# Optimization experiments

Measured on AMD Instinct MI355X. Metric: run time of the kernel, lower is better.

Reference implementation:

```python
import jax, jax.numpy as jnp
import numpy as np

HEAD_SIZE = 64
SCALE = HEAD_SIZE ** -0.5


def setup_inputs() -> dict:
    key = jax.random.key(0)
    ks = jax.random.split(key, 7)
    B, T, E, H = 32, 2048, 1024, HEAD_SIZE
    x = jax.random.normal(ks[0], (B, T, E), dtype=jnp.float32)
    Wq = jax.random.normal(ks[1], (E, H), dtype=jnp.float32) * (E ** -0.5)
    bq = jax.random.normal(ks[2], (H,), dtype=jnp.float32) * 0.02
    Wk = jax.random.normal(ks[3], (E, H), dtype=jnp.float32) * (E ** -0.5)
    bk = jax.random.normal(ks[4], (H,), dtype=jnp.float32) * 0.02
    Wv = jax.random.normal(ks[5], (E, H), dtype=jnp.float32) * (E ** -0.5)
    bv = jax.random.normal(ks[6], (H,), dtype=jnp.float32) * 0.02
    return {"x": x, "Wq": Wq, "bq": bq, "Wk": Wk, "bk": bk, "Wv": Wv, "bv": bv}


def reference(x, Wq, bq, Wk, bk, Wv, bv):
    # Faithful to the torch source: the tril buffer is all ones so the mask is a
    # no-op, and F.softmax's result is discarded. Output = (Q K^T * scale) @ V.
    Q = x @ Wq + bq          # [B, T, H]
    K = x @ Wk + bk          # [B, T, H]
    V = x @ Wv + bv          # [B, T, H]
    wei = jnp.einsum('bqh,bkh->bqk', Q, K) * SCALE  # [B, T, T]
    return jnp.einsum('bqk,bkh->bqh', wei, V)       # [B, T, H]
```

## Files before the change

### kernel.cpp

```cpp
#include <hip/hip_runtime.h>
#include <hip/hip_bf16.h>


using bf16x8 = __attribute__((ext_vector_type(8))) short;
using f32x4  = __attribute__((ext_vector_type(4))) float;
using u32x4  = __attribute__((ext_vector_type(4))) unsigned int;
using u32x2  = __attribute__((ext_vector_type(2))) unsigned int;
using u16    = unsigned short;

__device__ __forceinline__ u16 f2bf(float f) {
    unsigned u = __builtin_bit_cast(unsigned, f);
    u += 0x7fffu + ((u >> 16) & 1u);
    return (u16)(u >> 16);
}
__device__ __forceinline__ float bflo(unsigned u) { return __builtin_bit_cast(float, u << 16); }
__device__ __forceinline__ float bfhi(unsigned u) { return __builtin_bit_cast(float, u & 0xffff0000u); }

#define G2L16(g, l) __builtin_amdgcn_global_load_lds(                         \
    (const __attribute__((address_space(1))) void*)(g),                       \
    (__attribute__((address_space(3))) void*)(l), 16, 0, 0)

__global__ __launch_bounds__(256) void k_wt(const float* __restrict__ Wq,
                                            const float* __restrict__ Wk,
                                            const float* __restrict__ Wv,
                                            u16* __restrict__ WT) {
    const int n = blockIdx.x;
    const int seg = n >> 6, col = n & 63;
    const float* W = (seg == 0) ? Wq : (seg == 1) ? Wk : Wv;
    const int tid = threadIdx.x;
#pragma unroll
    for (int p = 0; p < 4; ++p) {
        const int e = tid + p * 256;
        WT[n * 1024 + e] = f2bf(W[e * 64 + col]);
    }
}

__global__ __launch_bounds__(512, 2) void k_qkv(const float* __restrict__ x,
                                                const u16* __restrict__ WT,
                                                const float* __restrict__ bq,
                                                const float* __restrict__ bk,
                                                const float* __restrict__ bv,
                                                u16* __restrict__ Qb,
                                                u16* __restrict__ Kb,
                                                u16* __restrict__ Vb) {
    __shared__ char lds[2 * 57344];
    const int tid  = threadIdx.x;
    const int wave = tid >> 6, lane = tid & 63;
    const int wr = wave >> 1, wc = wave & 1;
    const size_t row0 = (size_t)blockIdx.x * 128;

    size_t xsrc[4]; int xdst[4];
#pragma unroll
    for (int i = 0; i < 4; ++i) {
        const int r  = wave * 16 + i * 4 + (lane >> 4);
        const int cb = ((lane & 15) * 16) ^ ((r & 7) << 5);
        xsrc[i] = (row0 + r) * 1024 + (cb >> 2);
        xdst[i] = wave * 4096 + i * 1024;
    }
    size_t wsrc[3]; int wdst[3];
#pragma unroll
    for (int j = 0; j < 3; ++j) {
        const int n  = wave * 24 + j * 8 + (lane >> 3);
        const int cb = ((lane & 7) * 16) ^ ((n & 7) << 4);
        wsrc[j] = (size_t)n * 1024 + (cb >> 1);
        wdst[j] = 32768 + wave * 3072 + j * 1024;
    }

    f32x4 acc[2][6];
#pragma unroll
    for (int m = 0; m < 2; ++m)
#pragma unroll
        for (int n = 0; n < 6; ++n)
#pragma unroll
            for (int r = 0; r < 4; ++r) acc[m][n][r] = 0.0f;

#pragma unroll
    for (int i = 0; i < 4; ++i) G2L16(x + xsrc[i], lds + xdst[i]);
#pragma unroll
    for (int j = 0; j < 3; ++j) G2L16(WT + wsrc[j], lds + wdst[j]);

    for (int kc = 0; kc < 16; ++kc) {
        const int cur = kc & 1;
        if (kc < 15) {
            const int k0 = (kc + 1) * 64;
            char* base = lds + (cur ^ 1) * 57344;
#pragma unroll
            for (int i = 0; i < 4; ++i) G2L16(x + xsrc[i] + k0, base + xdst[i]);
#pragma unroll
            for (int j = 0; j < 3; ++j) G2L16(WT + wsrc[j] + k0, base + wdst[j]);
            asm volatile("s_waitcnt vmcnt(7)" ::: "memory");
        } else {
            asm volatile("s_waitcnt vmcnt(0)" ::: "memory");
        }
        __builtin_amdgcn_s_barrier();
        __builtin_amdgcn_sched_barrier(0);

        const char* xb = lds + cur * 57344;
        const char* wb = xb + 32768;
#pragma unroll
        for (int ks = 0; ks < 2; ++ks) {
            bf16x8 af[2];
#pragma unroll
            for (int m = 0; m < 2; ++m) {
                const int r = wr * 32 + m * 16 + (lane & 15);
                const int P = (r * 256 + ks * 128 + (lane >> 4) * 32) ^ ((r & 7) << 5);
                const f32x4 lo = *(const f32x4*)(xb + P);
                const f32x4 hi = *(const f32x4*)(xb + P + 16);
                u32x4 pk;
                pk[0] = (unsigned)f2bf(lo[0]) | ((unsigned)f2bf(lo[1]) << 16);
                pk[1] = (unsigned)f2bf(lo[2]) | ((unsigned)f2bf(lo[3]) << 16);
                pk[2] = (unsigned)f2bf(hi[0]) | ((unsigned)f2bf(hi[1]) << 16);
                pk[3] = (unsigned)f2bf(hi[2]) | ((unsigned)f2bf(hi[3]) << 16);
                af[m] = __builtin_bit_cast(bf16x8, pk);
            }
#pragma unroll
            for (int n = 0; n < 6; ++n) {
                const int nn = wc * 96 + n * 16 + (lane & 15);
                const int P  = (nn * 128 + ks * 64 + (lane >> 4) * 16) ^ ((nn & 7) << 4);
                const bf16x8 bfr = *(const bf16x8*)(wb + P);
                acc[0][n] = __builtin_amdgcn_mfma_f32_16x16x32_bf16(af[0], bfr, acc[0][n], 0, 0, 0);
                acc[1][n] = __builtin_amdgcn_mfma_f32_16x16x32_bf16(af[1], bfr, acc[1][n], 0, 0, 0);
            }
        }
        __builtin_amdgcn_sched_barrier(0);
        __builtin_amdgcn_s_barrier();
    }

#pragma unroll
    for (int n = 0; n < 6; ++n) {
        const int ncol = wc * 96 + n * 16 + (lane & 15);
        const int seg = ncol >> 6, col = ncol & 63;
        const float bias = ((seg == 0) ? bq : (seg == 1) ? bk : bv)[col];
        u16* const dst = (seg == 0) ? Qb : (seg == 1) ? Kb : Vb;
#pragma unroll
        for (int m = 0; m < 2; ++m) {
            const size_t rbase = row0 + wr * 32 + m * 16 + ((lane >> 4) << 2);
#pragma unroll
            for (int rr = 0; rr < 4; ++rr)
                dst[(rbase + rr) * 64 + col] = f2bf(acc[m][n][rr] + bias);
        }
    }
}

__global__ __launch_bounds__(256) void k_ktv(const u16* __restrict__ Kb,
                                             const u16* __restrict__ Vb,
                                             float* __restrict__ part) {
    __shared__ float Ks[64][68];
    __shared__ float Vs[64][68];
    const int tid = threadIdx.x;
    const int b = blockIdx.x >> 5, c = blockIdx.x & 31;
    const int i0 = (tid & 15) * 4;
    const int j0 = (tid >> 4) * 4;
    const int tr = tid >> 2, sc0 = (tid & 3) * 16;
    const size_t base = ((size_t)b * 2048 + c * 64) * 64;

    {
        const size_t src = base + (size_t)tr * 64 + sc0;
        const u32x4 ka = *(const u32x4*)(Kb + src);
        const u32x4 k2 = *(const u32x4*)(Kb + src + 8);
        const u32x4 va = *(const u32x4*)(Vb + src);
        const u32x4 v2 = *(const u32x4*)(Vb + src + 8);
        f32x4 t;
        t[0]=bflo(ka[0]); t[1]=bfhi(ka[0]); t[2]=bflo(ka[1]); t[3]=bfhi(ka[1]);
        *(f32x4*)&Ks[tr][sc0]      = t;
        t[0]=bflo(ka[2]); t[1]=bfhi(ka[2]); t[2]=bflo(ka[3]); t[3]=bfhi(ka[3]);
        *(f32x4*)&Ks[tr][sc0 + 4]  = t;
        t[0]=bflo(k2[0]); t[1]=bfhi(k2[0]); t[2]=bflo(k2[1]); t[3]=bfhi(k2[1]);
        *(f32x4*)&Ks[tr][sc0 + 8]  = t;
        t[0]=bflo(k2[2]); t[1]=bfhi(k2[2]); t[2]=bflo(k2[3]); t[3]=bfhi(k2[3]);
        *(f32x4*)&Ks[tr][sc0 + 12] = t;
        t[0]=bflo(va[0]); t[1]=bfhi(va[0]); t[2]=bflo(va[1]); t[3]=bfhi(va[1]);
        *(f32x4*)&Vs[tr][sc0]      = t;
        t[0]=bflo(va[2]); t[1]=bfhi(va[2]); t[2]=bflo(va[3]); t[3]=bfhi(va[3]);
        *(f32x4*)&Vs[tr][sc0 + 4]  = t;
        t[0]=bflo(v2[0]); t[1]=bfhi(v2[0]); t[2]=bflo(v2[1]); t[3]=bfhi(v2[1]);
        *(f32x4*)&Vs[tr][sc0 + 8]  = t;
        t[0]=bflo(v2[2]); t[1]=bfhi(v2[2]); t[2]=bflo(v2[3]); t[3]=bfhi(v2[3]);
        *(f32x4*)&Vs[tr][sc0 + 12] = t;
    }
    __syncthreads();

    f32x4 facc[4];
#pragma unroll
    for (int j = 0; j < 4; ++j)
#pragma unroll
        for (int q = 0; q < 4; ++q) facc[j][q] = 0.0f;

#pragma unroll 4
    for (int t = 0; t < 64; ++t) {
        const f32x4 kv = *(const f32x4*)&Ks[t][i0];
#pragma unroll
        for (int j = 0; j < 4; ++j) facc[j] += kv * Vs[t][j0 + j];
    }
    float* const P = part + (size_t)blockIdx.x * 4096;
#pragma unroll
    for (int j = 0; j < 4; ++j)
        *(f32x4*)&P[(j0 + j) * 64 + i0] = facc[j];
}

__global__ __launch_bounds__(256) void k_red(const float* __restrict__ part,
                                             u16* __restrict__ KtVT) {
    const int b = blockIdx.x >> 2;
    const int o0 = (blockIdx.x & 3) * 1024 + threadIdx.x * 4;
    const float* const Pb = part + (size_t)b * 32 * 4096;
    f32x4 s;
    s[0] = s[1] = s[2] = s[3] = 0.0f;
#pragma unroll 8
    for (int c = 0; c < 32; ++c) s += *(const f32x4*)(Pb + c * 4096 + o0);
    s *= 0.125f;
    u32x2 pk;
    pk[0] = (unsigned)f2bf(s[0]) | ((unsigned)f2bf(s[1]) << 16);
    pk[1] = (unsigned)f2bf(s[2]) | ((unsigned)f2bf(s[3]) << 16);
    *(u32x2*)(KtVT + (size_t)b * 4096 + o0) = pk;
}

__global__ __launch_bounds__(256) void k_out(const u16* __restrict__ Qb,
                                             const u16* __restrict__ KtVT,
                                             float* __restrict__ out) {
    const int tid = threadIdx.x;
    const int wave = tid >> 6, lane = tid & 63;
    const size_t m0 = (size_t)blockIdx.x * 64 + wave * 16;
    const int b = blockIdx.x >> 5;
    const u16* const Bp = KtVT + (size_t)b * 4096;

    bf16x8 bfrag[2][4];
#pragma unroll
    for (int ks = 0; ks < 2; ++ks)
#pragma unroll
        for (int nt = 0; nt < 4; ++nt)
            bfrag[ks][nt] = *(const bf16x8*)(Bp + (nt * 16 + (lane & 15)) * 64 + ks * 32 + (lane >> 4) * 8);

    f32x4 acc[4];
#pragma unroll
    for (int nt = 0; nt < 4; ++nt)
#pragma unroll
        for (int r = 0; r < 4; ++r) acc[nt][r] = 0.0f;

#pragma unroll
    for (int ks = 0; ks < 2; ++ks) {
        const bf16x8 a = *(const bf16x8*)(Qb + (m0 + (lane & 15)) * 64 + ks * 32 + (lane >> 4) * 8);
#pragma unroll
        for (int nt = 0; nt < 4; ++nt)
            acc[nt] = __builtin_amdgcn_mfma_f32_16x16x32_bf16(a, bfrag[ks][nt], acc[nt], 0, 0, 0);
    }
#pragma unroll
    for (int nt = 0; nt < 4; ++nt)
#pragma unroll
        for (int rr = 0; rr < 4; ++rr)
            out[(m0 + (lane >> 4) * 4 + rr) * 64 + nt * 16 + (lane & 15)] = acc[nt][rr];
}

extern "C" void kernel_launch(void* const* d_in, const int* in_sizes, int n_in,
                              void* d_out, int out_size, void* d_ws, size_t ws_size,
                              hipStream_t stream) {
    (void)in_sizes; (void)n_in; (void)out_size; (void)ws_size;
    const float* x  = (const float*)d_in[0];
    const float* Wq = (const float*)d_in[1];
    const float* bq = (const float*)d_in[2];
    const float* Wk = (const float*)d_in[3];
    const float* bk = (const float*)d_in[4];
    const float* Wv = (const float*)d_in[5];
    const float* bv = (const float*)d_in[6];
    float* out = (float*)d_out;

    char* ws = (char*)d_ws;
    u16*  WT   = (u16*)(ws);
    u16*  Qb   = (u16*)(ws + 0x60000);
    u16*  Kb   = (u16*)(ws + 0x860000);
    u16*  Vb   = (u16*)(ws + 0x1060000);
    float* part= (float*)(ws + 0x1860000);
    u16*  KtVT = (u16*)(ws + 0x2860000);

    k_wt <<<192,  256, 0, stream>>>(Wq, Wk, Wv, WT);
    k_qkv<<<512,  512, 0, stream>>>(x, WT, bq, bk, bv, Qb, Kb, Vb);
    k_ktv<<<1024, 256, 0, stream>>>(Kb, Vb, part);
    k_red<<<128,  256, 0, stream>>>(part, KtVT);
    k_out<<<1024, 256, 0, stream>>>(Qb, KtVT, out);
}
```

Measured before the change: 105.2 us.

## Fuse K^T V partial products into QKV projection kernel via LDS and MFMA

The QKV projection kernel now works on 64-row tiles and keeps K and V transposed in LDS instead of writing them to global memory. It then computes each tile's K^T V partial with MFMA and writes it straight to the partial buffer, which removes the separate k_ktv kernel and its K/V round trip. The weight transpose kernel is also rewritten to use a coalesced LDS transpose with vector stores. The tradeoff is more blocks with fewer accumulators each, a different LDS footprint and occupancy target, and a smaller MMA tile per block.

```diff
diff --git a/kernel.cpp b/kernel.cpp
--- a/kernel.cpp
+++ b/kernel.cpp
@@ -13,8 +13,6 @@
     u += 0x7fffu + ((u >> 16) & 1u);
     return (u16)(u >> 16);
 }
-__device__ __forceinline__ float bflo(unsigned u) { return __builtin_bit_cast(float, u << 16); }
-__device__ __forceinline__ float bfhi(unsigned u) { return __builtin_bit_cast(float, u & 0xffff0000u); }
 
 #define G2L16(g, l) __builtin_amdgcn_global_load_lds(                         \
     (const __attribute__((address_space(1))) void*)(g),                       \
@@ -24,58 +22,69 @@
                                             const float* __restrict__ Wk,
                                             const float* __restrict__ Wv,
                                             u16* __restrict__ WT) {
-    const int n = blockIdx.x;
-    const int seg = n >> 6, col = n & 63;
+    __shared__ float Wl[64][68];
+    const int seg = blockIdx.x >> 4, chunk = blockIdx.x & 15;
     const float* W = (seg == 0) ? Wq : (seg == 1) ? Wk : Wv;
+    const int e0 = chunk * 64;
     const int tid = threadIdx.x;
-#pragma unroll
-    for (int p = 0; p < 4; ++p) {
-        const int e = tid + p * 256;
-        WT[n * 1024 + e] = f2bf(W[e * 64 + col]);
-    }
-}
-
-__global__ __launch_bounds__(512, 2) void k_qkv(const float* __restrict__ x,
+    const int lr = tid >> 4, lc = (tid & 15) * 4;
+#pragma unroll
+    for (int p = 0; p < 4; ++p)
+        *(f32x4*)&Wl[lr + p * 16][lc] = *(const f32x4*)(W + (size_t)(e0 + lr + p * 16) * 64 + lc);
+    __syncthreads();
+    const int c = tid >> 2, eb = (tid & 3) * 16;
+    u32x4 o0, o1;
+#pragma unroll
+    for (int q = 0; q < 4; ++q)
+        o0[q] = (unsigned)f2bf(Wl[eb + 2 * q][c]) | ((unsigned)f2bf(Wl[eb + 2 * q + 1][c]) << 16);
+#pragma unroll
+    for (int q = 0; q < 4; ++q)
+        o1[q] = (unsigned)f2bf(Wl[eb + 8 + 2 * q][c]) | ((unsigned)f2bf(Wl[eb + 9 + 2 * q][c]) << 16);
+    u16* dst = WT + (size_t)(seg * 64 + c) * 1024 + e0 + eb;
+    *(u32x4*)dst = o0;
+    *(u32x4*)(dst + 8) = o1;
+}
+
+__global__ __launch_bounds__(512, 4) void k_qkv(const float* __restrict__ x,
                                                 const u16* __restrict__ WT,
                                                 const float* __restrict__ bq,
                                                 const float* __restrict__ bk,
                                                 const float* __restrict__ bv,
                                                 u16* __restrict__ Qb,
-                                                u16* __restrict__ Kb,
-                                                u16* __restrict__ Vb) {
-    __shared__ char lds[2 * 57344];
+                                                float* __restrict__ part) {
+    __shared__ __align__(16) char lds[81920];
     const int tid  = threadIdx.x;
     const int wave = tid >> 6, lane = tid & 63;
-    const int wr = wave >> 1, wc = wave & 1;
-    const size_t row0 = (size_t)blockIdx.x * 128;
-
-    size_t xsrc[4]; int xdst[4];
-#pragma unroll
-    for (int i = 0; i < 4; ++i) {
-        const int r  = wave * 16 + i * 4 + (lane >> 4);
-        const int cb = ((lane & 15) * 16) ^ ((r & 7) << 5);
+    const int wr = wave >> 2, wc = wave & 3;
+    const size_t row0 = (size_t)blockIdx.x * 64;
+
+    size_t xsrc[2]; int xdst[2];
+#pragma unroll
+    for (int i = 0; i < 2; ++i) {
+        const int r  = (tid >> 4) + i * 32;
+        const int cb = ((tid & 15) * 16) ^ ((r & 7) << 5);
         xsrc[i] = (row0 + r) * 1024 + (cb >> 2);
-        xdst[i] = wave * 4096 + i * 1024;
+        xdst[i] = i * 8192 + wave * 1024;
     }
     size_t wsrc[3]; int wdst[3];
 #pragma unroll
     for (int j = 0; j < 3; ++j) {
-        const int n  = wave * 24 + j * 8 + (lane >> 3);
-        const int cb = ((lane & 7) * 16) ^ ((n & 7) << 4);
+        const int n  = (tid >> 3) + j * 64;
+        const int cb = ((tid & 7) * 16) ^ ((n & 7) << 4);
         wsrc[j] = (size_t)n * 1024 + (cb >> 1);
-        wdst[j] = 32768 + wave * 3072 + j * 1024;
-    }
-
-    f32x4 acc[2][6];
+        wdst[j] = 16384 + j * 8192 + wave * 1024;
+    }
+
+    f32x4 acc[2][3];
 #pragma unroll
     for (int m = 0; m < 2; ++m)
 #pragma unroll
-        for (int n = 0; n < 6; ++n)
+        for (int n = 0; n < 3; ++n)
 #pragma unroll
             for (int r = 0; r < 4; ++r) acc[m][n][r] = 0.0f;
 
 #pragma unroll
-    for (int i = 0; i < 4; ++i) G2L16(x + xsrc[i], lds + xdst[i]);
+    for (int i = 0; i < 2; ++i) G2L16(x + xsrc[i], lds + xdst[i]);
 #pragma unroll
     for (int j = 0; j < 3; ++j) G2L16(WT + wsrc[j], lds + wdst[j]);
 
@@ -83,20 +92,20 @@
         const int cur = kc & 1;
         if (kc < 15) {
             const int k0 = (kc + 1) * 64;
-            char* base = lds + (cur ^ 1) * 57344;
-#pragma unroll
-            for (int i = 0; i < 4; ++i) G2L16(x + xsrc[i] + k0, base + xdst[i]);
+            char* base = lds + (cur ^ 1) * 40960;
+#pragma unroll
+            for (int i = 0; i < 2; ++i) G2L16(x + xsrc[i] + k0, base + xdst[i]);
 #pragma unroll
             for (int j = 0; j < 3; ++j) G2L16(WT + wsrc[j] + k0, base + wdst[j]);
-            asm volatile("s_waitcnt vmcnt(7)" ::: "memory");
+            asm volatile("s_waitcnt vmcnt(5)" ::: "memory");
         } else {
             asm volatile("s_waitcnt vmcnt(0)" ::: "memory");
         }
         __builtin_amdgcn_s_barrier();
         __builtin_amdgcn_sched_barrier(0);
 
-        const char* xb = lds + cur * 57344;
-        const char* wb = xb + 32768;
+        const char* xb = lds + cur * 40960;
+        const char* wb = xb + 16384;
 #pragma unroll
         for (int ks = 0; ks < 2; ++ks) {
             bf16x8 af[2];
@@ -114,8 +123,8 @@
                 af[m] = __builtin_bit_cast(bf16x8, pk);
             }
 #pragma unroll
-            for (int n = 0; n < 6; ++n) {
-                const int nn = wc * 96 + n * 16 + (lane & 15);
+            for (int n = 0; n < 3; ++n) {
+                const int nn = wc * 48 + n * 16 + (lane & 15);
                 const int P  = (nn * 128 + ks * 64 + (lane >> 4) * 16) ^ ((nn & 7) << 4);
                 const bf16x8 bfr = *(const bf16x8*)(wb + P);
                 acc[0][n] = __builtin_amdgcn_mfma_f32_16x16x32_bf16(af[0], bfr, acc[0][n], 0, 0, 0);
@@ -126,76 +135,49 @@
         __builtin_amdgcn_s_barrier();
     }
 
-#pragma unroll
-    for (int n = 0; n < 6; ++n) {
-        const int ncol = wc * 96 + n * 16 + (lane & 15);
-        const int seg = ncol >> 6, col = ncol & 63;
+    u16* const Kt = (u16*)lds;
+    u16* const Vt = (u16*)(lds + 16384);
+#pragma unroll
+    for (int n = 0; n < 3; ++n) {
+        const int ncol = wc * 48 + n * 16;
+        const int seg = ncol >> 6;
+        const int col = (ncol & 63) + (lane & 15);
         const float bias = ((seg == 0) ? bq : (seg == 1) ? bk : bv)[col];
-        u16* const dst = (seg == 0) ? Qb : (seg == 1) ? Kb : Vb;
 #pragma unroll
         for (int m = 0; m < 2; ++m) {
-            const size_t rbase = row0 + wr * 32 + m * 16 + ((lane >> 4) << 2);
-#pragma unroll
-            for (int rr = 0; rr < 4; ++rr)
-                dst[(rbase + rr) * 64 + col] = f2bf(acc[m][n][rr] + bias);
-        }
-    }
-}
-
-__global__ __launch_bounds__(256) void k_ktv(const u16* __restrict__ Kb,
-                                             const u16* __restrict__ Vb,
-                                             float* __restrict__ part) {
-    __shared__ float Ks[64][68];
-    __shared__ float Vs[64][68];
-    const int tid = threadIdx.x;
-    const int b = blockIdx.x >> 5, c = blockIdx.x & 31;
-    const int i0 = (tid & 15) * 4;
-    const int j0 = (tid >> 4) * 4;
-    const int tr = tid >> 2, sc0 = (tid & 3) * 16;
-    const size_t base = ((size_t)b * 2048 + c * 64) * 64;
-
-    {
-        const size_t src = base + (size_t)tr * 64 + sc0;
-        const u32x4 ka = *(const u32x4*)(Kb + src);
-        const u32x4 k2 = *(const u32x4*)(Kb + src + 8);
-        const u32x4 va = *(const u32x4*)(Vb + src);
-        const u32x4 v2 = *(const u32x4*)(Vb + src + 8);
-        f32x4 t;
-        t[0]=bflo(ka[0]); t[1]=bfhi(ka[0]); t[2]=bflo(ka[1]); t[3]=bfhi(ka[1]);
-        *(f32x4*)&Ks[tr][sc0]      = t;
-        t[0]=bflo(ka[2]); t[1]=bfhi(ka[2]); t[2]=bflo(ka[3]); t[3]=bfhi(ka[3]);
-        *(f32x4*)&Ks[tr][sc0 + 4]  = t;
-        t[0]=bflo(k2[0]); t[1]=bfhi(k2[0]); t[2]=bflo(k2[1]); t[3]=bfhi(k2[1]);
-        *(f32x4*)&Ks[tr][sc0 + 8]  = t;
-        t[0]=bflo(k2[2]); t[1]=bfhi(k2[2]); t[2]=bflo(k2[3]); t[3]=bfhi(k2[3]);
-        *(f32x4*)&Ks[tr][sc0 + 12] = t;
-        t[0]=bflo(va[0]); t[1]=bfhi(va[0]); t[2]=bflo(va[1]); t[3]=bfhi(va[1]);
-        *(f32x4*)&Vs[tr][sc0]      = t;
-        t[0]=bflo(va[2]); t[1]=bfhi(va[2]); t[2]=bflo(va[3]); t[3]=bfhi(va[3]);
-        *(f32x4*)&Vs[tr][sc0 + 4]  = t;
-        t[0]=bflo(v2[0]); t[1]=bfhi(v2[0]); t[2]=bflo(v2[1]); t[3]=bfhi(v2[1]);
-        *(f32x4*)&Vs[tr][sc0 + 8]  = t;
-        t[0]=bflo(v2[2]); t[1]=bfhi(v2[2]); t[2]=bflo(v2[3]); t[3]=bfhi(v2[3]);
-        *(f32x4*)&Vs[tr][sc0 + 12] = t;
+            const int rloc = wr * 32 + m * 16 + ((lane >> 4) << 2);
+            if (seg == 0) {
+#pragma unroll
+                for (int rr = 0; rr < 4; ++rr)
+                    Qb[(row0 + rloc + rr) * 64 + col] = f2bf(acc[m][n][rr] + bias);
+            } else {
+                u16* const T = (seg == 1) ? Kt : Vt;
+#pragma unroll
+                for (int rr = 0; rr < 4; ++rr)
+                    T[col * 72 + rloc + rr] = f2bf(acc[m][n][rr] + bias);
+            }
+        }
     }
     __syncthreads();
 
-    f32x4 facc[4];
-#pragma unroll
-    for (int j = 0; j < 4; ++j)
-#pragma unroll
-        for (int q = 0; q < 4; ++q) facc[j][q] = 0.0f;
-
-#pragma unroll 4
-    for (int t = 0; t < 64; ++t) {
-        const f32x4 kv = *(const f32x4*)&Ks[t][i0];
-#pragma unroll
-        for (int j = 0; j < 4; ++j) facc[j] += kv * Vs[t][j0 + j];
-    }
     float* const P = part + (size_t)blockIdx.x * 4096;
 #pragma unroll
-    for (int j = 0; j < 4; ++j)
-        *(f32x4*)&P[(j0 + j) * 64 + i0] = facc[j];
+    for (int i = 0; i < 2; ++i) {
+        const int f = wave * 2 + i;
+        const int m0 = (f & 3) * 16;
+        const int n0 = (f >> 2) * 16;
+        f32x4 d;
+        d[0] = d[1] = d[2] = d[3] = 0.0f;
+#pragma unroll
+        for (int ks = 0; ks < 2; ++ks) {
+            const bf16x8 a = *(const bf16x8*)(Vt + (m0 + (lane & 15)) * 72 + ks * 32 + (lane >> 4) * 8);
+            const bf16x8 b = *(const bf16x8*)(Kt + (n0 + (lane & 15)) * 72 + ks * 32 + (lane >> 4) * 8);
+            d = __builtin_amdgcn_mfma_f32_16x16x32_bf16(a, b, d, 0, 0, 0);
+        }
+#pragma unroll
+        for (int rr = 0; rr < 4; ++rr)
+            P[(m0 + (lane >> 4) * 4 + rr) * 64 + n0 + (lane & 15)] = d[rr];
+    }
 }
 
 __global__ __launch_bounds__(256) void k_red(const float* __restrict__ part,
@@ -266,14 +248,11 @@
     char* ws = (char*)d_ws;
     u16*  WT   = (u16*)(ws);
     u16*  Qb   = (u16*)(ws + 0x60000);
-    u16*  Kb   = (u16*)(ws + 0x860000);
-    u16*  Vb   = (u16*)(ws + 0x1060000);
-    float* part= (float*)(ws + 0x1860000);
-    u16*  KtVT = (u16*)(ws + 0x2860000);
-
-    k_wt <<<192,  256, 0, stream>>>(Wq, Wk, Wv, WT);
-    k_qkv<<<512,  512, 0, stream>>>(x, WT, bq, bk, bv, Qb, Kb, Vb);
-    k_ktv<<<1024, 256, 0, stream>>>(Kb, Vb, part);
+    float* part= (float*)(ws + 0x860000);
+    u16*  KtVT = (u16*)(ws + 0x1860000);
+
+    k_wt <<<48,   256, 0, stream>>>(Wq, Wk, Wv, WT);
+    k_qkv<<<1024, 512, 0, stream>>>(x, WT, bq, bk, bv, Qb, part);
     k_red<<<128,  256, 0, stream>>>(part, KtVT);
     k_out<<<1024, 256, 0, stream>>>(Qb, KtVT, out);
 }
```

Result: faster. 92.33 us (-12.2%).
